# Kernel optimization log

Measured on AMD Instinct MI355X. Metric: run time of the kernel, lower is better.

The kernel has to match this reference:

```python
import jax, jax.numpy as jnp
import numpy as np

H = 4  # attention heads

def _ln(x, g, b):
    m = jnp.mean(x, -1, keepdims=True)
    v = jnp.mean((x - m) ** 2, -1, keepdims=True)
    return (x - m) / jnp.sqrt(v + 1e-5) * g + b

def _gelu(x):
    return jax.nn.gelu(x, approximate=False)  # torch default GELU is exact erf

def _forward(node_states, edge_features,
             ee_w1, ee_b1, ee_ln_g, ee_ln_b, ee_w2, ee_b2,
             ts_w1, ts_b1, ts_ln_g, ts_ln_b, ts_w2, ts_b2, ts_w3, ts_b3,
             mc_w1, mc_b1, mc_ln_g, mc_ln_b, mc_w2, mc_b2,
             at_in_w, at_in_b, at_out_w, at_out_b,
             ag_w1, ag_b1, ag_ln_g, ag_ln_b, ag_w2, ag_b2,
             gt_w, gt_b, nn_ln_g, nn_ln_b, mn_ln_g, mn_ln_b):
    B, S, N, D = node_states.shape
    M = ee_w1.shape[1]
    hd = M // H
    # edge feature encoder: E -> M -> E (applied once to all edges)
    h = _gelu(_ln(edge_features @ ee_w1 + ee_b1, ee_ln_g, ee_ln_b))
    enc = h @ ee_w2 + ee_b2                       # [B,S,src,tgt,E]
    enc_t = jnp.moveaxis(enc, 3, 2)               # [B,S,tgt,src,E] (vectorizes the target-node loop)
    # transition strengths (gate per edge)
    t = _gelu(_ln(enc_t @ ts_w1 + ts_b1, ts_ln_g, ts_ln_b))
    t = _gelu(t @ ts_w2 + ts_b2)
    ts = jax.nn.sigmoid(t @ ts_w3 + ts_b3)        # [B,S,tgt,src,1]
    # message content: concat(source state, encoded edge feat) -> M
    src = jnp.broadcast_to(node_states[:, :, None, :, :], (B, S, N, N, D))
    mi = jnp.concatenate([src, enc_t], -1)        # [B,S,tgt,src,D+E]
    mh = _gelu(_ln(mi @ mc_w1 + mc_b1, mc_ln_g, mc_ln_b))
    msgs = mh @ mc_w2 + mc_b2                     # [B,S,tgt,src,M]
    wm = _ln(msgs * ts, mn_ln_g, mn_ln_b)         # weighted + message_norm
    # local self-attention over source-message dim per (b,s,target)
    qkv = wm @ at_in_w + at_in_b                  # [B,S,tgt,src,3M]
    q, k, v = jnp.split(qkv, 3, axis=-1)
    rh = lambda x: x.reshape(B, S, N, N, H, hd)
    q, k, v = rh(q), rh(k), rh(v)
    scores = jnp.einsum('bstqhd,bstkhd->bsthqk', q, k) / np.sqrt(hd).astype(np.float32)
    attn = jax.nn.softmax(scores, -1)
    ao = jnp.einsum('bsthqk,bstkhd->bstqhd', attn, v).reshape(B, S, N, N, M)
    ao = ao @ at_out_w + at_out_b
    agg = ao.mean(axis=3)                         # mean over source msgs -> [B,S,tgt,M]
    # aggregation MLP M -> D
    ni = _gelu(_ln(agg @ ag_w1 + ag_b1, ag_ln_g, ag_ln_b))
    ni = ni @ ag_w2 + ag_b2                       # [B,S,tgt,D]
    # gated update + node LayerNorm
    g = jax.nn.sigmoid(jnp.concatenate([node_states, ni], -1) @ gt_w + gt_b)
    upd = g * ni + (1.0 - g) * node_states
    return _ln(upd, nn_ln_g, nn_ln_b)             # [B,S,N,D]


def setup_inputs() -> dict:
    key = jax.random.key(0)
    B, S, N, D, E, M = 16, 128, 13, 128, 6, 64
    ks = iter(jax.random.split(key, 16))
    def lin(i, o):
        return jax.random.normal(next(ks), (i, o), jnp.float32) / np.float32(np.sqrt(i))
    z, o = jnp.zeros, jnp.ones
    return {
        'node_states': jax.random.normal(next(ks), (B, S, N, D), jnp.float32),
        'edge_features': jax.random.normal(next(ks), (B, S, N, N, E), jnp.float32),
        'ee_w1': lin(E, M), 'ee_b1': z(M), 'ee_ln_g': o(M), 'ee_ln_b': z(M),
        'ee_w2': lin(M, E), 'ee_b2': z(E),
        'ts_w1': lin(E, M), 'ts_b1': z(M), 'ts_ln_g': o(M), 'ts_ln_b': z(M),
        'ts_w2': lin(M, M // 2), 'ts_b2': z(M // 2), 'ts_w3': lin(M // 2, 1), 'ts_b3': z(1),
        'mc_w1': lin(D + E, M), 'mc_b1': z(M), 'mc_ln_g': o(M), 'mc_ln_b': z(M),
        'mc_w2': lin(M, M), 'mc_b2': z(M),
        'at_in_w': lin(M, 3 * M), 'at_in_b': z(3 * M), 'at_out_w': lin(M, M), 'at_out_b': z(M),
        'ag_w1': lin(M, D), 'ag_b1': z(D), 'ag_ln_g': o(D), 'ag_ln_b': z(D),
        'ag_w2': lin(D, D), 'ag_b2': z(D),
        'gt_w': lin(2 * D, D), 'gt_b': z(D),
        'nn_ln_g': o(D), 'nn_ln_b': z(D), 'mn_ln_g': o(M), 'mn_ln_b': z(M),
    }


def reference(node_states, edge_features,
              ee_w1, ee_b1, ee_ln_g, ee_ln_b, ee_w2, ee_b2,
              ts_w1, ts_b1, ts_ln_g, ts_ln_b, ts_w2, ts_b2, ts_w3, ts_b3,
              mc_w1, mc_b1, mc_ln_g, mc_ln_b, mc_w2, mc_b2,
              at_in_w, at_in_b, at_out_w, at_out_b,
              ag_w1, ag_b1, ag_ln_g, ag_ln_b, ag_w2, ag_b2,
              gt_w, gt_b, nn_ln_g, nn_ln_b, mn_ln_g, mn_ln_b):
    return _forward(node_states, edge_features,
                    ee_w1, ee_b1, ee_ln_g, ee_ln_b, ee_w2, ee_b2,
                    ts_w1, ts_b1, ts_ln_g, ts_ln_b, ts_w2, ts_b2, ts_w3, ts_b3,
                    mc_w1, mc_b1, mc_ln_g, mc_ln_b, mc_w2, mc_b2,
                    at_in_w, at_in_b, at_out_w, at_out_b,
                    ag_w1, ag_b1, ag_ln_g, ag_ln_b, ag_w2, ag_b2,
                    gt_w, gt_b, nn_ln_g, nn_ln_b, mn_ln_g, mn_ln_b)
```

## Files before the change

kernel.cpp:

```cpp
#include <hip/hip_runtime.h>

#define B_  16
#define S_  128
#define N_  13
#define D_  128
#define E_  6
#define M_  64
#define H_  4

typedef float v2f __attribute__((ext_vector_type(2)));
typedef float v4f __attribute__((ext_vector_type(4)));
typedef short v8s __attribute__((ext_vector_type(8)));

#define MFMA16(A, B, C) __builtin_amdgcn_mfma_f32_16x16x32_bf16((A), (B), (C), 0, 0, 0)
#define LDS_ORDER() __asm__ __volatile__("" ::: "memory")

#if __has_builtin(__builtin_elementwise_fma)
#define PKFMA(A, B, C) __builtin_elementwise_fma((A), (B), (C))
#else
#define PKFMA(A, B, C) ((A) * (B) + (C))
#endif
#define LO2(X) __builtin_shufflevector((X), (X), 0, 1)
#define HI2(X) __builtin_shufflevector((X), (X), 2, 3)

#define F_BTS   0
#define F_BMC   64
#define F_AOP   128
#define F_AG1P  4224
#define F_AG2P  12416
#define F_GTP   28800
#define F_TOTAL 61568
#define H_EE1   0
#define H_WTS   2048
#define H_TS2   6144
#define H_MC1   8192
#define H_WMCE  16384
#define H_MC2   20480
#define H_ATI   24576
#define H_TOTAL 36864

__device__ __forceinline__ v2f mkpair(float a, float b) { v2f r; r.x = a; r.y = b; return r; }

__device__ __forceinline__ unsigned short f2bs(float x) {
    unsigned u = __float_as_uint(x);
    u += 0x7FFFu + ((u >> 16) & 1u);
    return (unsigned short)(u >> 16);
}
__device__ __forceinline__ float erf_fast(float x) {
    float ax = fabsf(x);
    float t  = __builtin_amdgcn_rcpf(fmaf(0.3275911f, ax, 1.0f));
    float p  = t * fmaf(t, fmaf(t, fmaf(t, fmaf(t, 1.061405429f, -1.453152027f),
                                        1.421413741f), -0.284496736f), 0.254829592f);
    float r  = fmaf(-p, __expf(-ax * ax), 1.0f);
    return copysignf(r, x);
}
__device__ __forceinline__ float geluf(float x) {
    return 0.5f * x * (1.0f + erf_fast(x * 0.7071067811865475f));
}
__device__ __forceinline__ float sigm(float x) { return 1.0f / (1.0f + __expf(-x)); }
__device__ __forceinline__ v4f gelu4(v4f x) {
    v4f r; r[0] = geluf(x[0]); r[1] = geluf(x[1]); r[2] = geluf(x[2]); r[3] = geluf(x[3]);
    return r;
}

template <bool DOGELU>
__device__ __forceinline__ void ln_c64(v4f &a0, v4f &a1, v4f &a2, v4f &a3,
                                       float g0, float g1, float g2, float g3,
                                       float b0, float b1, float b2, float b3) {
    v4f s = a0 + a1 + a2 + a3;
    v4f q = a0 * a0 + a1 * a1 + a2 * a2 + a3 * a3;
#pragma unroll
    for (int o = 1; o < 16; o <<= 1) {
#pragma unroll
        for (int r = 0; r < 4; r++) {
            s[r] += __shfl_xor(s[r], o, 64);
            q[r] += __shfl_xor(q[r], o, 64);
        }
    }
    v4f mean = s * 0.015625f;
    v4f rs;
#pragma unroll
    for (int r = 0; r < 4; r++) {
        float var = fmaxf(q[r] * 0.015625f - mean[r] * mean[r], 0.f);
        rs[r] = rsqrtf(var + 1e-5f);
    }
    a0 = (a0 - mean) * rs * g0 + b0;
    a1 = (a1 - mean) * rs * g1 + b1;
    a2 = (a2 - mean) * rs * g2 + b2;
    a3 = (a3 - mean) * rs * g3 + b3;
    if (DOGELU) { a0 = gelu4(a0); a1 = gelu4(a1); a2 = gelu4(a2); a3 = gelu4(a3); }
}

template <bool DOGELU>
__device__ __forceinline__ void ln128(float &x0, float &x1, float g0_, float g1_,
                                      float b0_, float b1_) {
    float s = x0 + x1, q = x0 * x0 + x1 * x1;
#pragma unroll
    for (int o = 1; o < 64; o <<= 1) { s += __shfl_xor(s, o, 64); q += __shfl_xor(q, o, 64); }
    float mean = s * (1.f / 128.f);
    float var  = fmaxf(q * (1.f / 128.f) - mean * mean, 0.f);
    float rs   = rsqrtf(var + 1e-5f);
    x0 = (x0 - mean) * rs * g0_ + b0_;
    x1 = (x1 - mean) * rs * g1_ + b1_;
    if (DOGELU) { x0 = geluf(x0); x1 = geluf(x1); }
}

__device__ __forceinline__ void store_c(unsigned short (*xr)[136], int colbase, int L,
                                        v4f a0, v4f a1, v4f a2, v4f a3) {
    const int c = L & 15, g = L >> 4;
#pragma unroll
    for (int r = 0; r < 4; r++) {
        xr[4 * g + r][colbase + c]      = f2bs(a0[r]);
        xr[4 * g + r][colbase + 16 + c] = f2bs(a1[r]);
        xr[4 * g + r][colbase + 32 + c] = f2bs(a2[r]);
        xr[4 * g + r][colbase + 48 + c] = f2bs(a3[r]);
    }
}

__device__ __forceinline__ v8s pack8(v4f lo, v4f hi) {
    v8s r;
    r[0] = (short)f2bs(lo[0]); r[1] = (short)f2bs(lo[1]);
    r[2] = (short)f2bs(lo[2]); r[3] = (short)f2bs(lo[3]);
    r[4] = (short)f2bs(hi[0]); r[5] = (short)f2bs(hi[1]);
    r[6] = (short)f2bs(hi[2]); r[7] = (short)f2bs(hi[3]);
    return r;
}

struct Params {
    const float *node_states, *edge_features;
    const float *ee_w1, *ee_b1, *ee_ln_g, *ee_ln_b, *ee_w2, *ee_b2;
    const float *ts_w1, *ts_b1, *ts_ln_g, *ts_ln_b, *ts_w2, *ts_b2, *ts_w3, *ts_b3;
    const float *mc_w1, *mc_b1, *mc_ln_g, *mc_ln_b, *mc_w2, *mc_b2;
    const float *at_in_w, *at_in_b, *at_out_w, *at_out_b;
    const float *ag_w1, *ag_b1, *ag_ln_g, *ag_ln_b, *ag_w2, *ag_b2;
    const float *gt_w, *gt_b, *nn_ln_g, *nn_ln_b, *mn_ln_g, *mn_ln_b;
    float *ws;
    float *out;
};

__global__ __launch_bounds__(256) void prep_kernel(Params p) {
    int i = blockIdx.x * 256 + threadIdx.x;
    if (i < F_TOTAL) {
        float v;
        if (i < F_BMC) {
            int o = i - F_BTS;
            float s = p.ts_b1[o];
            for (int e = 0; e < E_; e++) s += p.ee_b2[e] * p.ts_w1[e * M_ + o];
            v = s;
        } else if (i < F_AOP) {
            int o = i - F_BMC;
            float s = p.mc_b1[o];
            for (int e = 0; e < E_; e++) s += p.ee_b2[e] * p.mc_w1[(D_ + e) * M_ + o];
            v = s;
        } else if (i < F_AG1P) {
            int x = i - F_AOP, r = x >> 2, kk = x & 3, k4 = r >> 6, ch = r & 63;
            v = p.at_out_w[(4 * k4 + kk) * M_ + ch];
        } else if (i < F_AG2P) {
            int x = i - F_AG1P, r = x >> 2, kk = x & 3, k4 = r >> 7, ch = r & 127;
            v = p.ag_w1[(4 * k4 + kk) * D_ + ch];
        } else if (i < F_GTP) {
            int x = i - F_AG2P, r = x >> 2, kk = x & 3, k4 = r >> 7, ch = r & 127;
            v = p.ag_w2[(4 * k4 + kk) * D_ + ch];
        } else {
            int x = i - F_GTP, r = x >> 2, kk = x & 3, k4 = r >> 7, ch = r & 127;
            v = p.gt_w[(4 * k4 + kk) * D_ + ch];
        }
        p.ws[i] = v;
        return;
    }
    int hi = i - F_TOTAL;
    if (hi >= H_TOTAL) return;
    unsigned short *wsh = (unsigned short *)(p.ws + F_TOTAL);
    int base, NT;
    const int region =
        (hi < H_WTS) ? 0 : (hi < H_TS2) ? 1 : (hi < H_MC1) ? 2 :
        (hi < H_WMCE) ? 3 : (hi < H_MC2) ? 4 : (hi < H_ATI) ? 5 : 6;
    switch (region) {
        case 0: base = H_EE1;  NT = 4;  break;
        case 1: base = H_WTS;  NT = 4;  break;
        case 2: base = H_TS2;  NT = 2;  break;
        case 3: base = H_MC1;  NT = 4;  break;
        case 4: base = H_WMCE; NT = 4;  break;
        case 5: base = H_MC2;  NT = 4;  break;
        default: base = H_ATI; NT = 12; break;
    }
    int r0 = hi - base;
    int j  = r0 & 7, L = (r0 >> 3) & 63, tk = r0 >> 9;
    int kc = tk / NT, T = tk - kc * NT;
    int c  = L & 15, gg = L >> 4;
    int k  = 32 * kc + 8 * gg + j;
    int n  = 16 * T + c;
    float v = 0.f;
    switch (region) {
        case 0: v = (k < E_) ? p.ee_w1[k * M_ + n] : 0.f; break;
        case 1: { float s = 0.f;
                  for (int e = 0; e < E_; e++) s += p.ee_w2[k * E_ + e] * p.ts_w1[e * M_ + n];
                  v = s; } break;
        case 2: v = p.ts_w2[k * 32 + n]; break;
        case 3: v = p.mc_w1[k * M_ + n]; break;
        case 4: { float s = 0.f;
                  for (int e = 0; e < E_; e++) s += p.ee_w2[k * E_ + e] * p.mc_w1[(D_ + e) * M_ + n];
                  v = s; } break;
        case 5: v = p.mc_w2[k * M_ + n]; break;
        default: v = p.at_in_w[k * 192 + n]; break;
    }
    wsh[hi] = f2bs(v);
}

#define SPL4(NAME, EXPR) v4f NAME; { float _b = (EXPR); NAME = (v4f){_b, _b, _b, _b}; }

__global__ __launch_bounds__(256) void petri_kernel(Params p) {
    const int tid = threadIdx.x;
    const int w   = tid >> 6;
    const int L   = tid & 63;
    const int c   = L & 15, g = L >> 4;
    const int taskA = blockIdx.x * 8 + w * 2;
    const int taskB = taskA + 1;
    const int bsA = taskA / N_, tA = taskA - bsA * N_;
    const int bsB = taskB / N_, tB = taskB - bsB * N_;
    const int mrow = (c < N_) ? c : 0;

    __shared__ __align__(16) unsigned short xp[4][2][16][136];
    float *xvA = (float *)&xp[w][0][0][0];
    float *xvB = (float *)&xp[w][1][0][0];

    const float *ws = p.ws;
    const v8s *wb = (const v8s *)((const unsigned short *)(ws + F_TOTAL));
    const v8s zf = {0, 0, 0, 0, 0, 0, 0, 0};

    v8s ahA0, ahA1, ahB0, ahB1;
    {
        v8s aA, aB;
        {
            const float *eA = p.edge_features + (((size_t)bsA * N_ + mrow) * N_ + tA) * E_;
            const float *eB = p.edge_features + (((size_t)bsB * N_ + mrow) * N_ + tB) * E_;
            v2f fa = ((const v2f *)eA)[0], fb = ((const v2f *)eA)[1], fc = ((const v2f *)eA)[2];
            v2f ga_ = ((const v2f *)eB)[0], gb = ((const v2f *)eB)[1], gc = ((const v2f *)eB)[2];
            v8s ta = zf, tb = zf;
            ta[0] = (short)f2bs(fa.x); ta[1] = (short)f2bs(fa.y);
            ta[2] = (short)f2bs(fb.x); ta[3] = (short)f2bs(fb.y);
            ta[4] = (short)f2bs(fc.x); ta[5] = (short)f2bs(fc.y);
            tb[0] = (short)f2bs(ga_.x); tb[1] = (short)f2bs(ga_.y);
            tb[2] = (short)f2bs(gb.x); tb[3] = (short)f2bs(gb.y);
            tb[4] = (short)f2bs(gc.x); tb[5] = (short)f2bs(gc.y);
            aA = (g == 0) ? ta : zf;
            aB = (g == 0) ? tb : zf;
        }
        float b0 = p.ee_b1[c], b1 = p.ee_b1[16 + c], b2 = p.ee_b1[32 + c], b3 = p.ee_b1[48 + c];
        v4f h0A = {b0, b0, b0, b0}, h1A = {b1, b1, b1, b1}, h2A = {b2, b2, b2, b2}, h3A = {b3, b3, b3, b3};
        v4f h0B = h0A, h1B = h1A, h2B = h2A, h3B = h3A;
        {
            v8s W0 = wb[0 * 64 + L], W1 = wb[1 * 64 + L], W2 = wb[2 * 64 + L], W3 = wb[3 * 64 + L];
            h0A = MFMA16(aA, W0, h0A); h0B = MFMA16(aB, W0, h0B);
            h1A = MFMA16(aA, W1, h1A); h1B = MFMA16(aB, W1, h1B);
            h2A = MFMA16(aA, W2, h2A); h2B = MFMA16(aB, W2, h2B);
            h3A = MFMA16(aA, W3, h3A); h3B = MFMA16(aB, W3, h3B);
        }
        float lg0 = p.ee_ln_g[c], lg1 = p.ee_ln_g[16 + c], lg2 = p.ee_ln_g[32 + c], lg3 = p.ee_ln_g[48 + c];
        float lb0 = p.ee_ln_b[c], lb1 = p.ee_ln_b[16 + c], lb2 = p.ee_ln_b[32 + c], lb3 = p.ee_ln_b[48 + c];
        ln_c64<true>(h0A, h1A, h2A, h3A, lg0, lg1, lg2, lg3, lb0, lb1, lb2, lb3);
        ln_c64<true>(h0B, h1B, h2B, h3B, lg0, lg1, lg2, lg3, lb0, lb1, lb2, lb3);
        store_c(xp[w][0], 64, L, h0A, h1A, h2A, h3A);
        store_c(xp[w][1], 64, L, h0B, h1B, h2B, h3B);
        LDS_ORDER();
        ahA0 = *(const v8s *)&xp[w][0][c][64 + 8 * g];
        ahA1 = *(const v8s *)&xp[w][0][c][96 + 8 * g];
        ahB0 = *(const v8s *)&xp[w][1][c][64 + 8 * g];
        ahB1 = *(const v8s *)&xp[w][1][c][96 + 8 * g];
    }

    v4f tsvA, tsvB;
    {
        float b0 = ws[F_BTS + c], b1 = ws[F_BTS + 16 + c], b2 = ws[F_BTS + 32 + c], b3 = ws[F_BTS + 48 + c];
        v4f t0A = {b0, b0, b0, b0}, t1A = {b1, b1, b1, b1}, t2A = {b2, b2, b2, b2}, t3A = {b3, b3, b3, b3};
        v4f t0B = t0A, t1B = t1A, t2B = t2A, t3B = t3A;
        {
            v8s W;
            W = wb[256 + 0 * 64 + L]; t0A = MFMA16(ahA0, W, t0A); t0B = MFMA16(ahB0, W, t0B);
            W = wb[256 + 4 * 64 + L]; t0A = MFMA16(ahA1, W, t0A); t0B = MFMA16(ahB1, W, t0B);
            W = wb[256 + 1 * 64 + L]; t1A = MFMA16(ahA0, W, t1A); t1B = MFMA16(ahB0, W, t1B);
            W = wb[256 + 5 * 64 + L]; t1A = MFMA16(ahA1, W, t1A); t1B = MFMA16(ahB1, W, t1B);
            W = wb[256 + 2 * 64 + L]; t2A = MFMA16(ahA0, W, t2A); t2B = MFMA16(ahB0, W, t2B);
            W = wb[256 + 6 * 64 + L]; t2A = MFMA16(ahA1, W, t2A); t2B = MFMA16(ahB1, W, t2B);
            W = wb[256 + 3 * 64 + L]; t3A = MFMA16(ahA0, W, t3A); t3B = MFMA16(ahB0, W, t3B);
            W = wb[256 + 7 * 64 + L]; t3A = MFMA16(ahA1, W, t3A); t3B = MFMA16(ahB1, W, t3B);
        }
        float lg0 = p.ts_ln_g[c], lg1 = p.ts_ln_g[16 + c], lg2 = p.ts_ln_g[32 + c], lg3 = p.ts_ln_g[48 + c];
        float lb0 = p.ts_ln_b[c], lb1 = p.ts_ln_b[16 + c], lb2 = p.ts_ln_b[32 + c], lb3 = p.ts_ln_b[48 + c];
        ln_c64<true>(t0A, t1A, t2A, t3A, lg0, lg1, lg2, lg3, lb0, lb1, lb2, lb3);
        ln_c64<true>(t0B, t1B, t2B, t3B, lg0, lg1, lg2, lg3, lb0, lb1, lb2, lb3);
        store_c(xp[w][0], 0, L, t0A, t1A, t2A, t3A);
        store_c(xp[w][1], 0, L, t0B, t1B, t2B, t3B);
        LDS_ORDER();
        v8s atA0 = *(const v8s *)&xp[w][0][c][0 + 8 * g];
        v8s atA1 = *(const v8s *)&xp[w][0][c][32 + 8 * g];
        v8s atB0 = *(const v8s *)&xp[w][1][c][0 + 8 * g];
        v8s atB1 = *(const v8s *)&xp[w][1][c][32 + 8 * g];
        float u0b = p.ts_b2[c], u1b = p.ts_b2[16 + c];
        v4f u0A = {u0b, u0b, u0b, u0b}, u1A = {u1b, u1b, u1b, u1b};
        v4f u0B = u0A, u1B = u1A;
        {
            v8s W;
            W = wb[768 + 0 * 64 + L]; u0A = MFMA16(atA0, W, u0A); u0B = MFMA16(atB0, W, u0B);
            W = wb[768 + 2 * 64 + L]; u0A = MFMA16(atA1, W, u0A); u0B = MFMA16(atB1, W, u0B);
            W = wb[768 + 1 * 64 + L]; u1A = MFMA16(atA0, W, u1A); u1B = MFMA16(atB0, W, u1B);
            W = wb[768 + 3 * 64 + L]; u1A = MFMA16(atA1, W, u1A); u1B = MFMA16(atB1, W, u1B);
        }
        float w3a = p.ts_w3[c], w3b = p.ts_w3[16 + c], b3v = p.ts_b3[0];
        v4f dA = gelu4(u0A) * w3a + gelu4(u1A) * w3b;
        v4f dB = gelu4(u0B) * w3a + gelu4(u1B) * w3b;
// ... 125 lines not shown
            aq = (g < 2) ? *(const v8s *)&xp[w][TI][c][16 + 8 * g] : zf;          \
            bk = (g < 2) ? *(const v8s *)&xp[w][TI][c][64 + 16 + 8 * g] : zf;     \
            s1 = MFMA16(aq, bk, z4);                                              \
            aq = (g < 2) ? *(const v8s *)&xp[w][TI][c][32 + 8 * g] : zf;          \
            bk = (g < 2) ? *(const v8s *)&xp[w][TI][c][64 + 32 + 8 * g] : zf;     \
            s2 = MFMA16(aq, bk, z4);                                              \
            aq = (g < 2) ? *(const v8s *)&xp[w][TI][c][48 + 8 * g] : zf;          \
            bk = (g < 2) ? *(const v8s *)&xp[w][TI][c][64 + 48 + 8 * g] : zf;     \
            s3 = MFMA16(aq, bk, z4);                                              \
        }                                                                         \
        if (c >= N_) {                                                            \
            v4f neg = {-1e30f, -1e30f, -1e30f, -1e30f};                           \
            s0 = neg; s1 = neg; s2 = neg; s3 = neg;                               \
        }                                                                         \
        v4f m0 = s0, m1 = s1, m2 = s2, m3 = s3;                                   \
        _Pragma("unroll")                                                         \
        for (int o = 1; o < 16; o <<= 1)                                          \
            _Pragma("unroll")                                                     \
            for (int r = 0; r < 4; r++) {                                         \
                m0[r] = fmaxf(m0[r], __shfl_xor(m0[r], o, 64));                   \
                m1[r] = fmaxf(m1[r], __shfl_xor(m1[r], o, 64));                   \
                m2[r] = fmaxf(m2[r], __shfl_xor(m2[r], o, 64));                   \
                m3[r] = fmaxf(m3[r], __shfl_xor(m3[r], o, 64));                   \
            }                                                                     \
        v4f e0, e1, e2, e3;                                                       \
        _Pragma("unroll")                                                         \
        for (int r = 0; r < 4; r++) {                                             \
            e0[r] = __expf((s0[r] - m0[r]) * 0.25f);                              \
            e1[r] = __expf((s1[r] - m1[r]) * 0.25f);                              \
            e2[r] = __expf((s2[r] - m2[r]) * 0.25f);                              \
            e3[r] = __expf((s3[r] - m3[r]) * 0.25f);                              \
        }                                                                         \
        v4f z0 = e0, z1 = e1, z2 = e2, z3 = e3;                                   \
        _Pragma("unroll")                                                         \
        for (int o = 1; o < 16; o <<= 1)                                          \
            _Pragma("unroll")                                                     \
            for (int r = 0; r < 4; r++) {                                         \
                z0[r] += __shfl_xor(z0[r], o, 64);                                \
                z1[r] += __shfl_xor(z1[r], o, 64);                                \
                z2[r] += __shfl_xor(z2[r], o, 64);                                \
                z3[r] += __shfl_xor(z3[r], o, 64);                                \
            }                                                                     \
        _Pragma("unroll")                                                         \
        for (int r = 0; r < 4; r++) {                                             \
            e0[r] *= __builtin_amdgcn_rcpf(z0[r]);                                \
            e1[r] *= __builtin_amdgcn_rcpf(z1[r]);                                \
            e2[r] *= __builtin_amdgcn_rcpf(z2[r]);                                \
            e3[r] *= __builtin_amdgcn_rcpf(z3[r]);                                \
        }                                                                         \
        int row0 = 4 * g;                                                         \
        float cs0 = e0[0], cs1 = e1[0], cs2 = e2[0], cs3 = e3[0];                 \
        _Pragma("unroll")                                                         \
        for (int r = 1; r < 4; r++) {                                             \
            bool ok = (row0 + r) < N_;                                            \
            cs0 += ok ? e0[r] : 0.f; cs1 += ok ? e1[r] : 0.f;                     \
            cs2 += ok ? e2[r] : 0.f; cs3 += ok ? e3[r] : 0.f;                     \
        }                                                                         \
        cs0 += __shfl_xor(cs0, 16, 64); cs0 += __shfl_xor(cs0, 32, 64);           \
        cs1 += __shfl_xor(cs1, 16, 64); cs1 += __shfl_xor(cs1, 32, 64);           \
        cs2 += __shfl_xor(cs2, 16, 64); cs2 += __shfl_xor(cs2, 32, 64);           \
        cs3 += __shfl_xor(cs3, 16, 64); cs3 += __shfl_xor(cs3, 32, 64);           \
        int pbase = (((L & 48) + ((L & 48) >> 2)) << 2);                          \
        O0 = 0.f; O1 = 0.f; O2 = 0.f; O3 = 0.f;                                   \
        _Pragma("unroll")                                                         \
        for (int r = 0; r < 4; r++) {                                             \
            int pa = pbase + 4 * r;                                               \
            float c0 = __int_as_float(__builtin_amdgcn_ds_bpermute(pa, __float_as_int(cs0))); \
            float c1 = __int_as_float(__builtin_amdgcn_ds_bpermute(pa, __float_as_int(cs1))); \
            float c2 = __int_as_float(__builtin_amdgcn_ds_bpermute(pa, __float_as_int(cs2))); \
            float c3 = __int_as_float(__builtin_amdgcn_ds_bpermute(pa, __float_as_int(cs3))); \
            O0 += c0 * VT0[r]; O1 += c1 * VT1[r];                                 \
            O2 += c2 * VT2[r]; O3 += c3 * VT3[r];                                 \
        }                                                                         \
        O0 += __shfl_xor(O0, 16, 64); O0 += __shfl_xor(O0, 32, 64);               \
        O1 += __shfl_xor(O1, 16, 64); O1 += __shfl_xor(O1, 32, 64);               \
        O2 += __shfl_xor(O2, 16, 64); O2 += __shfl_xor(O2, 32, 64);               \
        O3 += __shfl_xor(O3, 16, 64); O3 += __shfl_xor(O3, 32, 64);               \
        const float inv13 = 1.0f / 13.0f;                                         \
        O0 *= inv13; O1 *= inv13; O2 *= inv13; O3 *= inv13;                       \
    }
    ATTN(0, vtA0, vtA1, vtA2, vtA3, agA0, agA1, agA2, agA3)
    ATTN(1, vtB0, vtB1, vtB2, vtB3, agB0, agB1, agB2, agB3)
#undef ATTN
    LDS_ORDER();

    if (g == 0) {
        xvA[c] = agA0; xvA[16 + c] = agA1; xvA[32 + c] = agA2; xvA[48 + c] = agA3;
        xvB[c] = agB0; xvB[16 + c] = agB1; xvB[32 + c] = agB2; xvB[48 + c] = agB3;
    }
    LDS_ORDER();
    {
        const v4f *AO = (const v4f *)(ws + F_AOP);
        v2f spA = mkpair(p.at_out_b[L], 0.f), spB = spA;
#pragma unroll 4
        for (int k4 = 0; k4 < 16; k4++) {
            v4f wv = AO[k4 * 64 + L];
            v4f xA = *(const v4f *)&xvA[4 * k4];
            v4f xB = *(const v4f *)&xvB[4 * k4];
            spA = PKFMA(LO2(xA), LO2(wv), PKFMA(HI2(xA), HI2(wv), spA));
            spB = PKFMA(LO2(xB), LO2(wv), PKFMA(HI2(xB), HI2(wv), spB));
        }
        xvA[64 + L] = spA.x + spA.y;
        xvB[64 + L] = spB.x + spB.y;
    }
    LDS_ORDER();
    {
        const v4f *AG = (const v4f *)(ws + F_AG1P);
        float bb0 = p.ag_b1[L], bb1 = p.ag_b1[L + 64];
        v2f pA0 = mkpair(bb0, 0.f), pA1 = mkpair(bb1, 0.f);
        v2f pB0 = pA0, pB1 = pA1;
#pragma unroll 4
        for (int k4 = 0; k4 < 16; k4++) {
            v4f w0 = AG[k4 * 128 + L], w1 = AG[k4 * 128 + 64 + L];
            v4f xA = *(const v4f *)&xvA[64 + 4 * k4];
            v4f xB = *(const v4f *)&xvB[64 + 4 * k4];
            pA0 = PKFMA(LO2(xA), LO2(w0), PKFMA(HI2(xA), HI2(w0), pA0));
            pA1 = PKFMA(LO2(xA), LO2(w1), PKFMA(HI2(xA), HI2(w1), pA1));
            pB0 = PKFMA(LO2(xB), LO2(w0), PKFMA(HI2(xB), HI2(w0), pB0));
            pB1 = PKFMA(LO2(xB), LO2(w1), PKFMA(HI2(xB), HI2(w1), pB1));
        }
        float aA0 = pA0.x + pA0.y, aA1 = pA1.x + pA1.y;
        float aB0 = pB0.x + pB0.y, aB1 = pB1.x + pB1.y;
        float lg0 = p.ag_ln_g[L], lg1 = p.ag_ln_g[L + 64];
        float lb0 = p.ag_ln_b[L], lb1 = p.ag_ln_b[L + 64];
        ln128<true>(aA0, aA1, lg0, lg1, lb0, lb1);
        ln128<true>(aB0, aB1, lg0, lg1, lb0, lb1);
        xvA[128 + L] = aA0; xvA[192 + L] = aA1;
        xvB[128 + L] = aB0; xvB[192 + L] = aB1;
    }
    LDS_ORDER();
    float nivA0, nivA1, nivB0, nivB1;
    {
        const v4f *AG = (const v4f *)(ws + F_AG2P);
        float bb0 = p.ag_b2[L], bb1 = p.ag_b2[L + 64];
        v2f pA0 = mkpair(bb0, 0.f), pA1 = mkpair(bb1, 0.f);
        v2f pB0 = pA0, pB1 = pA1;
#pragma unroll 8
        for (int k4 = 0; k4 < 32; k4++) {
            v4f w0 = AG[k4 * 128 + L], w1 = AG[k4 * 128 + 64 + L];
            v4f xA = *(const v4f *)&xvA[128 + 4 * k4];
            v4f xB = *(const v4f *)&xvB[128 + 4 * k4];
            pA0 = PKFMA(LO2(xA), LO2(w0), PKFMA(HI2(xA), HI2(w0), pA0));
            pA1 = PKFMA(LO2(xA), LO2(w1), PKFMA(HI2(xA), HI2(w1), pA1));
            pB0 = PKFMA(LO2(xB), LO2(w0), PKFMA(HI2(xB), HI2(w0), pB0));
            pB1 = PKFMA(LO2(xB), LO2(w1), PKFMA(HI2(xB), HI2(w1), pB1));
        }
        nivA0 = pA0.x + pA0.y; nivA1 = pA1.x + pA1.y;
        nivB0 = pB0.x + pB0.y; nivB1 = pB1.x + pB1.y;
    }
    const float *nstA = p.node_states + ((size_t)bsA * N_ + tA) * D_;
    const float *nstB = p.node_states + ((size_t)bsB * N_ + tB) * D_;
    float nA0 = nstA[L], nA1 = nstA[L + 64];
    float nB0 = nstB[L], nB1 = nstB[L + 64];
    xvA[L] = nA0; xvA[64 + L] = nA1;
    xvA[128 + L] = nivA0; xvA[192 + L] = nivA1;
    xvB[L] = nB0; xvB[64 + L] = nB1;
    xvB[128 + L] = nivB0; xvB[192 + L] = nivB1;
    LDS_ORDER();
    float updA0, updA1, updB0, updB1;
    {
        const v4f *GT = (const v4f *)(ws + F_GTP);
        float bb0 = p.gt_b[L], bb1 = p.gt_b[L + 64];
        v2f pA0 = mkpair(bb0, 0.f), pA1 = mkpair(bb1, 0.f);
        v2f pB0 = pA0, pB1 = pA1;
#pragma unroll 8
        for (int k4 = 0; k4 < 64; k4++) {
            v4f w0 = GT[k4 * 128 + L], w1 = GT[k4 * 128 + 64 + L];
            v4f xA = *(const v4f *)&xvA[4 * k4];
            v4f xB = *(const v4f *)&xvB[4 * k4];
            pA0 = PKFMA(LO2(xA), LO2(w0), PKFMA(HI2(xA), HI2(w0), pA0));
            pA1 = PKFMA(LO2(xA), LO2(w1), PKFMA(HI2(xA), HI2(w1), pA1));
            pB0 = PKFMA(LO2(xB), LO2(w0), PKFMA(HI2(xB), HI2(w0), pB0));
            pB1 = PKFMA(LO2(xB), LO2(w1), PKFMA(HI2(xB), HI2(w1), pB1));
        }
        float gA0 = sigm(pA0.x + pA0.y), gA1 = sigm(pA1.x + pA1.y);
        float gB0 = sigm(pB0.x + pB0.y), gB1 = sigm(pB1.x + pB1.y);
        updA0 = gA0 * nivA0 + (1.f - gA0) * nA0;
        updA1 = gA1 * nivA1 + (1.f - gA1) * nA1;
        updB0 = gB0 * nivB0 + (1.f - gB0) * nB0;
        updB1 = gB1 * nivB1 + (1.f - gB1) * nB1;
    }
    {
        float lg0 = p.nn_ln_g[L], lg1 = p.nn_ln_g[L + 64];
        float lb0 = p.nn_ln_b[L], lb1 = p.nn_ln_b[L + 64];
        ln128<false>(updA0, updA1, lg0, lg1, lb0, lb1);
        ln128<false>(updB0, updB1, lg0, lg1, lb0, lb1);
        float *opA = p.out + ((size_t)bsA * N_ + tA) * D_;
        float *opB = p.out + ((size_t)bsB * N_ + tB) * D_;
        opA[L] = updA0; opA[L + 64] = updA1;
        opB[L] = updB0; opB[L + 64] = updB1;
    }
}

extern "C" void kernel_launch(void* const* d_in, const int* in_sizes, int n_in,
                              void* d_out, int out_size, void* d_ws, size_t ws_size,
                              hipStream_t stream) {
    Params p;
    p.node_states   = (const float*)d_in[0];
    p.edge_features = (const float*)d_in[1];
    p.ee_w1   = (const float*)d_in[2];
    p.ee_b1   = (const float*)d_in[3];
    p.ee_ln_g = (const float*)d_in[4];
    p.ee_ln_b = (const float*)d_in[5];
    p.ee_w2   = (const float*)d_in[6];
    p.ee_b2   = (const float*)d_in[7];
    p.ts_w1   = (const float*)d_in[8];
    p.ts_b1   = (const float*)d_in[9];
    p.ts_ln_g = (const float*)d_in[10];
    p.ts_ln_b = (const float*)d_in[11];
    p.ts_w2   = (const float*)d_in[12];
    p.ts_b2   = (const float*)d_in[13];
    p.ts_w3   = (const float*)d_in[14];
    p.ts_b3   = (const float*)d_in[15];
    p.mc_w1   = (const float*)d_in[16];
    p.mc_b1   = (const float*)d_in[17];
    p.mc_ln_g = (const float*)d_in[18];
    p.mc_ln_b = (const float*)d_in[19];
    p.mc_w2   = (const float*)d_in[20];
    p.mc_b2   = (const float*)d_in[21];
    p.at_in_w  = (const float*)d_in[22];
    p.at_in_b  = (const float*)d_in[23];
    p.at_out_w = (const float*)d_in[24];
    p.at_out_b = (const float*)d_in[25];
    p.ag_w1   = (const float*)d_in[26];
    p.ag_b1   = (const float*)d_in[27];
    p.ag_ln_g = (const float*)d_in[28];
    p.ag_ln_b = (const float*)d_in[29];
    p.ag_w2   = (const float*)d_in[30];
    p.ag_b2   = (const float*)d_in[31];
    p.gt_w    = (const float*)d_in[32];
    p.gt_b    = (const float*)d_in[33];
    p.nn_ln_g = (const float*)d_in[34];
    p.nn_ln_b = (const float*)d_in[35];
    p.mn_ln_g = (const float*)d_in[36];
    p.mn_ln_b = (const float*)d_in[37];
    p.ws      = (float*)d_ws;
    p.out     = (float*)d_out;

    const int prep_threads = F_TOTAL + H_TOTAL;
    hipLaunchKernelGGL(prep_kernel, dim3((prep_threads + 255) / 256), dim3(256), 0, stream, p);
    hipLaunchKernelGGL(petri_kernel, dim3((B_ * S_ * N_) / 8), dim3(256), 0, stream, p);
}
```

Before: 391.9 us.

## Move per-node tail GEMMs to split-bf16 MFMA across the whole block

The node-level tail (attention out-projection, aggregation MLP, gate projection) used to run as per-wave packed FP32 FMA loops over two tasks each, with weights streamed from global memory. It now gathers the 8 tasks of the block into a shared 16-row tile and runs MFMA 16x16x32 bf16. Weights and activations are split into bf16 hi/lo parts, and three MFMAs per product keep accuracy close to FP32. This needs block-wide __syncthreads between stages and a new hi/lo weight layout from prep_kernel. Half of the 16 rows are padding, and the extra conversion work and LDS traffic add cost.

```diff
diff --git a/kernel.cpp b/kernel.cpp
--- a/kernel.cpp
+++ b/kernel.cpp
@@ -15,21 +15,18 @@
 #define MFMA16(A, B, C) __builtin_amdgcn_mfma_f32_16x16x32_bf16((A), (B), (C), 0, 0, 0)
 #define LDS_ORDER() __asm__ __volatile__("" ::: "memory")
 
-#if __has_builtin(__builtin_elementwise_fma)
-#define PKFMA(A, B, C) __builtin_elementwise_fma((A), (B), (C))
-#else
-#define PKFMA(A, B, C) ((A) * (B) + (C))
-#endif
-#define LO2(X) __builtin_shufflevector((X), (X), 0, 1)
-#define HI2(X) __builtin_shufflevector((X), (X), 2, 3)
-
 #define F_BTS   0
 #define F_BMC   64
 #define F_AOP   128
-#define F_AG1P  4224
-#define F_AG2P  12416
-#define F_GTP   28800
 #define F_TOTAL 61568
+#define NW_AOH  0
+#define NW_AOL  4096
+#define NW_AG1H 8192
+#define NW_AG1L 16384
+#define NW_AG2H 24576
+#define NW_AG2L 40960
+#define NW_GTH  57344
+#define NW_GTL  90112
 #define H_EE1   0
 #define H_WTS   2048
 #define H_TS2   6144
@@ -39,12 +36,13 @@
 #define H_ATI   24576
 #define H_TOTAL 36864
 
-__device__ __forceinline__ v2f mkpair(float a, float b) { v2f r; r.x = a; r.y = b; return r; }
-
 __device__ __forceinline__ unsigned short f2bs(float x) {
     unsigned u = __float_as_uint(x);
     u += 0x7FFFu + ((u >> 16) & 1u);
     return (unsigned short)(u >> 16);
+}
+__device__ __forceinline__ float bs2f(unsigned short h) {
+    return __uint_as_float((unsigned)h << 16);
 }
 __device__ __forceinline__ float erf_fast(float x) {
     float ax = fabsf(x);
@@ -124,6 +122,12 @@
     r[4] = (short)f2bs(hi[0]); r[5] = (short)f2bs(hi[1]);
     r[6] = (short)f2bs(hi[2]); r[7] = (short)f2bs(hi[3]);
     return r;
+}
+
+__device__ __forceinline__ void wr_hl(unsigned short *ph, unsigned short *pl, float v) {
+    unsigned short h = f2bs(v);
+    *ph = h;
+    *pl = f2bs(v - bs2f(h));
 }
 
 struct Params {
@@ -140,32 +144,39 @@
 
 __global__ __launch_bounds__(256) void prep_kernel(Params p) {
     int i = blockIdx.x * 256 + threadIdx.x;
-    if (i < F_TOTAL) {
+    if (i < 128) {
         float v;
         if (i < F_BMC) {
             int o = i - F_BTS;
             float s = p.ts_b1[o];
             for (int e = 0; e < E_; e++) s += p.ee_b2[e] * p.ts_w1[e * M_ + o];
             v = s;
-        } else if (i < F_AOP) {
+        } else {
             int o = i - F_BMC;
             float s = p.mc_b1[o];
             for (int e = 0; e < E_; e++) s += p.ee_b2[e] * p.mc_w1[(D_ + e) * M_ + o];
             v = s;
-        } else if (i < F_AG1P) {
-            int x = i - F_AOP, r = x >> 2, kk = x & 3, k4 = r >> 6, ch = r & 63;
-            v = p.at_out_w[(4 * k4 + kk) * M_ + ch];
-        } else if (i < F_AG2P) {
-            int x = i - F_AG1P, r = x >> 2, kk = x & 3, k4 = r >> 7, ch = r & 127;
-            v = p.ag_w1[(4 * k4 + kk) * D_ + ch];
-        } else if (i < F_GTP) {
-            int x = i - F_AG2P, r = x >> 2, kk = x & 3, k4 = r >> 7, ch = r & 127;
-            v = p.ag_w2[(4 * k4 + kk) * D_ + ch];
-        } else {
-            int x = i - F_GTP, r = x >> 2, kk = x & 3, k4 = r >> 7, ch = r & 127;
-            v = p.gt_w[(4 * k4 + kk) * D_ + ch];
         }
         p.ws[i] = v;
+        return;
+    }
+    if (i < F_TOTAL) {
+        int x = i - 128;
+        const float *W; int N, lsh, base, size;
+        if (x < 4096)       {             W = p.at_out_w; N = 64;  lsh = 2; base = NW_AOH;  size = 4096;  }
+        else if (x < 12288) { x -= 4096;  W = p.ag_w1;    N = 128; lsh = 3; base = NW_AG1H; size = 8192;  }
+        else if (x < 28672) { x -= 12288; W = p.ag_w2;    N = 128; lsh = 3; base = NW_AG2H; size = 16384; }
+        else                { x -= 28672; W = p.gt_w;     N = 128; lsh = 3; base = NW_GTH;  size = 32768; }
+        int j = x & 7, L = (x >> 3) & 63, t = x >> 9;
+        int kc = t >> lsh, nt = t & ((1 << lsh) - 1);
+        int k = 32 * kc + 8 * (L >> 4) + j;
+        int n = 16 * nt + (L & 15);
+        float v = W[k * N + n];
+        unsigned short h = f2bs(v);
+        unsigned short l = f2bs(v - bs2f(h));
+        unsigned short *NW = (unsigned short *)(p.ws + F_AOP);
+        NW[base + x]        = h;
+        NW[base + size + x] = l;
         return;
     }
     int hi = i - F_TOTAL;
@@ -207,8 +218,6 @@
     wsh[hi] = f2bs(v);
 }
 
-#define SPL4(NAME, EXPR) v4f NAME; { float _b = (EXPR); NAME = (v4f){_b, _b, _b, _b}; }
-
 __global__ __launch_bounds__(256) void petri_kernel(Params p) {
     const int tid = threadIdx.x;
     const int w   = tid >> 6;
@@ -221,11 +230,12 @@
     const int mrow = (c < N_) ? c : 0;
 
     __shared__ __align__(16) unsigned short xp[4][2][16][136];
-    float *xvA = (float *)&xp[w][0][0][0];
-    float *xvB = (float *)&xp[w][1][0][0];
+    unsigned short *xn = &xp[0][0][0][0];
+#define XNP(b, pl, r, col) (xn + (b) * 8448 + (pl) * 4224 + (r) * 264 + (col))
 
     const float *ws = p.ws;
     const v8s *wb = (const v8s *)((const unsigned short *)(ws + F_TOTAL));
+    const unsigned short *NW = (const unsigned short *)(ws + F_AOP);
     const v8s zf = {0, 0, 0, 0, 0, 0, 0, 0};
 
     v8s ahA0, ahA1, ahB0, ahB1;
@@ -517,105 +527,154 @@
     ATTN(0, vtA0, vtA1, vtA2, vtA3, agA0, agA1, agA2, agA3)
     ATTN(1, vtB0, vtB1, vtB2, vtB3, agB0, agB1, agB2, agB3)
 #undef ATTN
-    LDS_ORDER();
-
+
+    const int rA = 2 * w, rB = rA + 1;
+
+    __syncthreads();
     if (g == 0) {
-        xvA[c] = agA0; xvA[16 + c] = agA1; xvA[32 + c] = agA2; xvA[48 + c] = agA3;
-        xvB[c] = agB0; xvB[16 + c] = agB1; xvB[32 + c] = agB2; xvB[48 + c] = agB3;
-    }
-    LDS_ORDER();
-    {
-        const v4f *AO = (const v4f *)(ws + F_AOP);
-        v2f spA = mkpair(p.at_out_b[L], 0.f), spB = spA;
-#pragma unroll 4
-        for (int k4 = 0; k4 < 16; k4++) {
-            v4f wv = AO[k4 * 64 + L];
-            v4f xA = *(const v4f *)&xvA[4 * k4];
-            v4f xB = *(const v4f *)&xvB[4 * k4];
-            spA = PKFMA(LO2(xA), LO2(wv), PKFMA(HI2(xA), HI2(wv), spA));
-            spB = PKFMA(LO2(xB), LO2(wv), PKFMA(HI2(xB), HI2(wv), spB));
-        }
-        xvA[64 + L] = spA.x + spA.y;
-        xvB[64 + L] = spB.x + spB.y;
-    }
-    LDS_ORDER();
-    {
-        const v4f *AG = (const v4f *)(ws + F_AG1P);
-        float bb0 = p.ag_b1[L], bb1 = p.ag_b1[L + 64];
-        v2f pA0 = mkpair(bb0, 0.f), pA1 = mkpair(bb1, 0.f);
-        v2f pB0 = pA0, pB1 = pA1;
-#pragma unroll 4
-        for (int k4 = 0; k4 < 16; k4++) {
-            v4f w0 = AG[k4 * 128 + L], w1 = AG[k4 * 128 + 64 + L];
-            v4f xA = *(const v4f *)&xvA[64 + 4 * k4];
-            v4f xB = *(const v4f *)&xvB[64 + 4 * k4];
-            pA0 = PKFMA(LO2(xA), LO2(w0), PKFMA(HI2(xA), HI2(w0), pA0));
-            pA1 = PKFMA(LO2(xA), LO2(w1), PKFMA(HI2(xA), HI2(w1), pA1));
-            pB0 = PKFMA(LO2(xB), LO2(w0), PKFMA(HI2(xB), HI2(w0), pB0));
-            pB1 = PKFMA(LO2(xB), LO2(w1), PKFMA(HI2(xB), HI2(w1), pB1));
-        }
-        float aA0 = pA0.x + pA0.y, aA1 = pA1.x + pA1.y;
-        float aB0 = pB0.x + pB0.y, aB1 = pB1.x + pB1.y;
+        wr_hl(XNP(0, 0, rA, c),      XNP(0, 1, rA, c),      agA0);
+        wr_hl(XNP(0, 0, rA, 16 + c), XNP(0, 1, rA, 16 + c), agA1);
+        wr_hl(XNP(0, 0, rA, 32 + c), XNP(0, 1, rA, 32 + c), agA2);
+        wr_hl(XNP(0, 0, rA, 48 + c), XNP(0, 1, rA, 48 + c), agA3);
+        wr_hl(XNP(0, 0, rB, c),      XNP(0, 1, rB, c),      agB0);
+        wr_hl(XNP(0, 0, rB, 16 + c), XNP(0, 1, rB, 16 + c), agB1);
+        wr_hl(XNP(0, 0, rB, 32 + c), XNP(0, 1, rB, 32 + c), agB2);
+        wr_hl(XNP(0, 0, rB, 48 + c), XNP(0, 1, rB, 48 + c), agB3);
+    }
+    __syncthreads();
+
+    {
+        const v8s *WH = (const v8s *)(NW + NW_AOH);
+        const v8s *WL = (const v8s *)(NW + NW_AOL);
+        float bb = p.at_out_b[16 * w + c];
+        v4f acc = {bb, bb, bb, bb};
+#pragma unroll
+        for (int kc = 0; kc < 2; kc++) {
+            v8s xh = *(const v8s *)XNP(0, 0, c, 8 * g + 32 * kc);
+            v8s xl = *(const v8s *)XNP(0, 1, c, 8 * g + 32 * kc);
+            v8s wh = WH[(kc * 4 + w) * 64 + L];
+            v8s wl = WL[(kc * 4 + w) * 64 + L];
+            acc = MFMA16(xh, wl, acc);
+            acc = MFMA16(xl, wh, acc);
+            acc = MFMA16(xh, wh, acc);
+        }
+#pragma unroll
+        for (int r = 0; r < 4; r++)
+            wr_hl(XNP(1, 0, 4 * g + r, 16 * w + c), XNP(1, 1, 4 * g + r, 16 * w + c), acc[r]);
+    }
+    __syncthreads();
+
+    {
+        const v8s *WH = (const v8s *)(NW + NW_AG1H);
+        const v8s *WL = (const v8s *)(NW + NW_AG1L);
+        const int nt0 = 2 * w, nt1 = nt0 + 1;
+        float b0 = p.ag_b1[16 * nt0 + c], b1 = p.ag_b1[16 * nt1 + c];
+        v4f a0 = {b0, b0, b0, b0}, a1 = {b1, b1, b1, b1};
+#pragma unroll
+        for (int kc = 0; kc < 2; kc++) {
+            v8s xh = *(const v8s *)XNP(1, 0, c, 8 * g + 32 * kc);
+            v8s xl = *(const v8s *)XNP(1, 1, c, 8 * g + 32 * kc);
+            v8s wh0 = WH[(kc * 8 + nt0) * 64 + L], wl0 = WL[(kc * 8 + nt0) * 64 + L];
+            v8s wh1 = WH[(kc * 8 + nt1) * 64 + L], wl1 = WL[(kc * 8 + nt1) * 64 + L];
+            a0 = MFMA16(xh, wl0, a0); a1 = MFMA16(xh, wl1, a1);
+            a0 = MFMA16(xl, wh0, a0); a1 = MFMA16(xl, wh1, a1);
+            a0 = MFMA16(xh, wh0, a0); a1 = MFMA16(xh, wh1, a1);
+        }
+#pragma unroll
+        for (int r = 0; r < 4; r++) {
+            wr_hl(XNP(0, 0, 4 * g + r, 16 * nt0 + c), XNP(0, 1, 4 * g + r, 16 * nt0 + c), a0[r]);
+            wr_hl(XNP(0, 0, 4 * g + r, 16 * nt1 + c), XNP(0, 1, 4 * g + r, 16 * nt1 + c), a1[r]);
+        }
+    }
+    __syncthreads();
+
+    {
+        float xA0 = bs2f(*XNP(0, 0, rA, L))      + bs2f(*XNP(0, 1, rA, L));
+        float xA1 = bs2f(*XNP(0, 0, rA, 64 + L)) + bs2f(*XNP(0, 1, rA, 64 + L));
+        float xB0 = bs2f(*XNP(0, 0, rB, L))      + bs2f(*XNP(0, 1, rB, L));
+        float xB1 = bs2f(*XNP(0, 0, rB, 64 + L)) + bs2f(*XNP(0, 1, rB, 64 + L));
         float lg0 = p.ag_ln_g[L], lg1 = p.ag_ln_g[L + 64];
         float lb0 = p.ag_ln_b[L], lb1 = p.ag_ln_b[L + 64];
-        ln128<true>(aA0, aA1, lg0, lg1, lb0, lb1);
-        ln128<true>(aB0, aB1, lg0, lg1, lb0, lb1);
-        xvA[128 + L] = aA0; xvA[192 + L] = aA1;
-        xvB[128 + L] = aB0; xvB[192 + L] = aB1;
-    }
-    LDS_ORDER();
-    float nivA0, nivA1, nivB0, nivB1;
-    {
-        const v4f *AG = (const v4f *)(ws + F_AG2P);
-        float bb0 = p.ag_b2[L], bb1 = p.ag_b2[L + 64];
-        v2f pA0 = mkpair(bb0, 0.f), pA1 = mkpair(bb1, 0.f);
-        v2f pB0 = pA0, pB1 = pA1;
-#pragma unroll 8
-        for (int k4 = 0; k4 < 32; k4++) {
-            v4f w0 = AG[k4 * 128 + L], w1 = AG[k4 * 128 + 64 + L];
-            v4f xA = *(const v4f *)&xvA[128 + 4 * k4];
-            v4f xB = *(const v4f *)&xvB[128 + 4 * k4];
-            pA0 = PKFMA(LO2(xA), LO2(w0), PKFMA(HI2(xA), HI2(w0), pA0));
-            pA1 = PKFMA(LO2(xA), LO2(w1), PKFMA(HI2(xA), HI2(w1), pA1));
-            pB0 = PKFMA(LO2(xB), LO2(w0), PKFMA(HI2(xB), HI2(w0), pB0));
-            pB1 = PKFMA(LO2(xB), LO2(w1), PKFMA(HI2(xB), HI2(w1), pB1));
-        }
-        nivA0 = pA0.x + pA0.y; nivA1 = pA1.x + pA1.y;
-        nivB0 = pB0.x + pB0.y; nivB1 = pB1.x + pB1.y;
-    }
+        ln128<true>(xA0, xA1, lg0, lg1, lb0, lb1);
+        ln128<true>(xB0, xB1, lg0, lg1, lb0, lb1);
+        wr_hl(XNP(1, 0, rA, L),      XNP(1, 1, rA, L),      xA0);
+        wr_hl(XNP(1, 0, rA, 64 + L), XNP(1, 1, rA, 64 + L), xA1);
+        wr_hl(XNP(1, 0, rB, L),      XNP(1, 1, rB, L),      xB0);
+        wr_hl(XNP(1, 0, rB, 64 + L), XNP(1, 1, rB, 64 + L), xB1);
+    }
+    __syncthreads();
+
     const float *nstA = p.node_states + ((size_t)bsA * N_ + tA) * D_;
     const float *nstB = p.node_states + ((size_t)bsB * N_ + tB) * D_;
     float nA0 = nstA[L], nA1 = nstA[L + 64];
     float nB0 = nstB[L], nB1 = nstB[L + 64];
-    xvA[L] = nA0; xvA[64 + L] = nA1;
-    xvA[128 + L] = nivA0; xvA[192 + L] = nivA1;
-    xvB[L] = nB0; xvB[64 + L] = nB1;
-    xvB[128 + L] = nivB0; xvB[192 + L] = nivB1;
-    LDS_ORDER();
-    float updA0, updA1, updB0, updB1;
-    {
-        const v4f *GT = (const v4f *)(ws + F_GTP);
-        float bb0 = p.gt_b[L], bb1 = p.gt_b[L + 64];
-        v2f pA0 = mkpair(bb0, 0.f), pA1 = mkpair(bb1, 0.f);
-        v2f pB0 = pA0, pB1 = pA1;
-#pragma unroll 8
-        for (int k4 = 0; k4 < 64; k4++) {
-            v4f w0 = GT[k4 * 128 + L], w1 = GT[k4 * 128 + 64 + L];
-            v4f xA = *(const v4f *)&xvA[4 * k4];
-            v4f xB = *(const v4f *)&xvB[4 * k4];
-            pA0 = PKFMA(LO2(xA), LO2(w0), PKFMA(HI2(xA), HI2(w0), pA0));
-            pA1 = PKFMA(LO2(xA), LO2(w1), PKFMA(HI2(xA), HI2(w1), pA1));
-            pB0 = PKFMA(LO2(xB), LO2(w0), PKFMA(HI2(xB), HI2(w0), pB0));
-            pB1 = PKFMA(LO2(xB), LO2(w1), PKFMA(HI2(xB), HI2(w1), pB1));
-        }
-        float gA0 = sigm(pA0.x + pA0.y), gA1 = sigm(pA1.x + pA1.y);
-        float gB0 = sigm(pB0.x + pB0.y), gB1 = sigm(pB1.x + pB1.y);
-        updA0 = gA0 * nivA0 + (1.f - gA0) * nA0;
-        updA1 = gA1 * nivA1 + (1.f - gA1) * nA1;
-        updB0 = gB0 * nivB0 + (1.f - gB0) * nB0;
-        updB1 = gB1 * nivB1 + (1.f - gB1) * nB1;
-    }
-    {
+    {
+        const v8s *WH = (const v8s *)(NW + NW_AG2H);
+        const v8s *WL = (const v8s *)(NW + NW_AG2L);
+        const int nt0 = 2 * w, nt1 = nt0 + 1;
+        float b0 = p.ag_b2[16 * nt0 + c], b1 = p.ag_b2[16 * nt1 + c];
+        v4f a0 = {b0, b0, b0, b0}, a1 = {b1, b1, b1, b1};
+#pragma unroll
+        for (int kc = 0; kc < 4; kc++) {
+            v8s xh = *(const v8s *)XNP(1, 0, c, 8 * g + 32 * kc);
+            v8s xl = *(const v8s *)XNP(1, 1, c, 8 * g + 32 * kc);
+            v8s wh0 = WH[(kc * 8 + nt0) * 64 + L], wl0 = WL[(kc * 8 + nt0) * 64 + L];
+            v8s wh1 = WH[(kc * 8 + nt1) * 64 + L], wl1 = WL[(kc * 8 + nt1) * 64 + L];
+            a0 = MFMA16(xh, wl0, a0); a1 = MFMA16(xh, wl1, a1);
+            a0 = MFMA16(xl, wh0, a0); a1 = MFMA16(xl, wh1, a1);
+            a0 = MFMA16(xh, wh0, a0); a1 = MFMA16(xh, wh1, a1);
+        }
+#pragma unroll
+        for (int r = 0; r < 4; r++) {
+            wr_hl(XNP(0, 0, 4 * g + r, 128 + 16 * nt0 + c), XNP(0, 1, 4 * g + r, 128 + 16 * nt0 + c), a0[r]);
+            wr_hl(XNP(0, 0, 4 * g + r, 128 + 16 * nt1 + c), XNP(0, 1, 4 * g + r, 128 + 16 * nt1 + c), a1[r]);
+        }
+        wr_hl(XNP(0, 0, rA, L),      XNP(0, 1, rA, L),      nA0);
+        wr_hl(XNP(0, 0, rA, 64 + L), XNP(0, 1, rA, 64 + L), nA1);
+        wr_hl(XNP(0, 0, rB, L),      XNP(0, 1, rB, L),      nB0);
+        wr_hl(XNP(0, 0, rB, 64 + L), XNP(0, 1, rB, 64 + L), nB1);
+    }
+    __syncthreads();
+
+    {
+        const v8s *WH = (const v8s *)(NW + NW_GTH);
+        const v8s *WL = (const v8s *)(NW + NW_GTL);
+        const int nt0 = 2 * w, nt1 = nt0 + 1;
+        float b0 = p.gt_b[16 * nt0 + c], b1 = p.gt_b[16 * nt1 + c];
+        v4f a0 = {b0, b0, b0, b0}, a1 = {b1, b1, b1, b1};
+#pragma unroll
+        for (int kc = 0; kc < 8; kc++) {
+            v8s xh = *(const v8s *)XNP(0, 0, c, 8 * g + 32 * kc);
+            v8s xl = *(const v8s *)XNP(0, 1, c, 8 * g + 32 * kc);
+            v8s wh0 = WH[(kc * 8 + nt0) * 64 + L], wl0 = WL[(kc * 8 + nt0) * 64 + L];
+            v8s wh1 = WH[(kc * 8 + nt1) * 64 + L], wl1 = WL[(kc * 8 + nt1) * 64 + L];
+            a0 = MFMA16(xh, wl0, a0); a1 = MFMA16(xh, wl1, a1);
+            a0 = MFMA16(xl, wh0, a0); a1 = MFMA16(xl, wh1, a1);
+            a0 = MFMA16(xh, wh0, a0); a1 = MFMA16(xh, wh1, a1);
+        }
+#pragma unroll
+        for (int r = 0; r < 4; r++) {
+            wr_hl(XNP(1, 0, 4 * g + r, 16 * nt0 + c), XNP(1, 1, 4 * g + r, 16 * nt0 + c), a0[r]);
+            wr_hl(XNP(1, 0, 4 * g + r, 16 * nt1 + c), XNP(1, 1, 4 * g + r, 16 * nt1 + c), a1[r]);
+        }
+    }
+    __syncthreads();
+
+    {
+        float gpA0 = bs2f(*XNP(1, 0, rA, L))      + bs2f(*XNP(1, 1, rA, L));
+        float gpA1 = bs2f(*XNP(1, 0, rA, 64 + L)) + bs2f(*XNP(1, 1, rA, 64 + L));
+        float gpB0 = bs2f(*XNP(1, 0, rB, L))      + bs2f(*XNP(1, 1, rB, L));
+        float gpB1 = bs2f(*XNP(1, 0, rB, 64 + L)) + bs2f(*XNP(1, 1, rB, 64 + L));
+        float niA0 = bs2f(*XNP(0, 0, rA, 128 + L)) + bs2f(*XNP(0, 1, rA, 128 + L));
+        float niA1 = bs2f(*XNP(0, 0, rA, 192 + L)) + bs2f(*XNP(0, 1, rA, 192 + L));
+        float niB0 = bs2f(*XNP(0, 0, rB, 128 + L)) + bs2f(*XNP(0, 1, rB, 128 + L));
+        float niB1 = bs2f(*XNP(0, 0, rB, 192 + L)) + bs2f(*XNP(0, 1, rB, 192 + L));
+        float gA0 = sigm(gpA0), gA1 = sigm(gpA1);
+        float gB0 = sigm(gpB0), gB1 = sigm(gpB1);
+        float updA0 = gA0 * niA0 + (1.f - gA0) * nA0;
+        float updA1 = gA1 * niA1 + (1.f - gA1) * nA1;
+        float updB0 = gB0 * niB0 + (1.f - gB0) * nB0;
+        float updB1 = gB1 * niB1 + (1.f - gB1) * nB1;
         float lg0 = p.nn_ln_g[L], lg1 = p.nn_ln_g[L + 64];
         float lb0 = p.nn_ln_b[L], lb1 = p.nn_ln_b[L + 64];
         ln128<false>(updA0, updA1, lg0, lg1, lb0, lb1);
@@ -625,6 +684,7 @@
         opA[L] = updA0; opA[L + 64] = updA1;
         opB[L] = updB0; opB[L + 64] = updB1;
     }
+#undef XNP
 }
 
 extern "C" void kernel_launch(void* const* d_in, const int* in_sizes, int n_in,
```

Result: faster. 357.8 us (-8.7%).
